# Optimization experiments

Hardware: AMD Instinct MI355X
Metric: run time of the kernel (lower is better)

## Reference

```python
import jax, jax.numpy as jnp
import numpy as np

IN_F, D_FC, D_H = 5, 32, 64

def setup_inputs() -> dict:
    key = jax.random.key(0)
    ks = jax.random.split(key, 10)
    B, T = 4096, 512
    s_fc = 1.0 / np.sqrt(IN_F)
    s_rnn = 1.0 / np.sqrt(D_H)
    s_out = 1.0 / np.sqrt(D_H)
    return {
        "x":    jax.random.normal(ks[0], (B, T, IN_F), dtype=jnp.float32),
        "W0":   jax.random.uniform(ks[1], (D_FC, IN_F), jnp.float32, -s_fc, s_fc),
        "b0":   jax.random.uniform(ks[2], (D_FC,), jnp.float32, -s_fc, s_fc),
        "W_ih": jax.random.uniform(ks[3], (4 * D_H, D_FC), jnp.float32, -s_rnn, s_rnn),
        "W_hh": jax.random.uniform(ks[4], (4 * D_H, D_H), jnp.float32, -s_rnn, s_rnn),
        "b_ih": jax.random.uniform(ks[5], (4 * D_H,), jnp.float32, -s_rnn, s_rnn),
        "b_hh": jax.random.uniform(ks[6], (4 * D_H,), jnp.float32, -s_rnn, s_rnn),
        "Wo":   jax.random.uniform(ks[7], (1, D_H), jnp.float32, -s_out, s_out),
        "bo":   jax.random.uniform(ks[8], (1,), jnp.float32, -s_out, s_out),
    }

def reference(x, W0, b0, W_ih, W_hh, b_ih, b_hh, Wo, bo):
    B, T, _ = x.shape
    # fc0: [B,T,5] -> [B,T,32]
    h0 = x @ W0.T + b0
    # Precompute input-side gate projections for all timesteps: [B,T,4H]
    xg = h0 @ W_ih.T + (b_ih + b_hh)
    xg_t = jnp.swapaxes(xg, 0, 1)  # [T,B,4H] for scan

    def step(carry, xg_step):
        h, c = carry
        gates = xg_step + h @ W_hh.T          # [B,4H]
        i, f, g, o = jnp.split(gates, 4, axis=-1)  # PyTorch gate order i,f,g,o
        i = jax.nn.sigmoid(i)
        f = jax.nn.sigmoid(f)
        g = jnp.tanh(g)
        o = jax.nn.sigmoid(o)
        c = f * c + i * g
        h = o * jnp.tanh(c)
        return (h, c), None

    init = (jnp.zeros((B, D_H), x.dtype), jnp.zeros((B, D_H), x.dtype))
    (h_last, _), _ = jax.lax.scan(step, init, xg_t)
    # out Linear on last timestep hidden: r_out[:, -1, :] == h_last
    return h_last @ Wo.T + bo  # [B,1]
```

## Files before the change

### kernel.cpp

```cpp
#include <hip/hip_runtime.h>

#define B_TOT   4096
#define T_STEPS 512
#define IN_F    5
#define D_FC    32
#define D_H     64
#define MB      16
#define NROW    16
#define ROWE    72

typedef _Float16 h8 __attribute__((ext_vector_type(8)));
typedef __fp16   h2 __attribute__((ext_vector_type(2)));
typedef float    f4 __attribute__((ext_vector_type(4)));

__device__ __forceinline__ float fexp2(float x) { return __builtin_amdgcn_exp2f(x); }
__device__ __forceinline__ float frcp(float x)  { return __builtin_amdgcn_rcpf(x); }

__global__ __launch_bounds__(256) void lstm_mfma(
    const float* __restrict__ x,
    const float* __restrict__ W0,
    const float* __restrict__ b0,
    const float* __restrict__ W_ih,
    const float* __restrict__ W_hh,
    const float* __restrict__ b_ih,
    const float* __restrict__ b_hh,
    const float* __restrict__ Wo,
    const float* __restrict__ bo,
    float* __restrict__ out)
{
    __shared__ __align__(16) _Float16 H[2][NROW][ROWE];

    const int tid  = threadIdx.x;
    const int lane = tid & 63;
    const int w    = tid >> 6;
    const int col  = lane & 15;
    const int quad = lane >> 4;
    const int bblk = blockIdx.x * MB;

    const float K1 = 1.4426950408889634f;
    const float K2 = 2.8853900817779268f;

    h8 Bf[4][2];
    #pragma unroll
    for (int q = 0; q < 4; ++q) {
        const int row = q * 64 + w * 16 + col;
        #pragma unroll
        for (int c = 0; c < 2; ++c) {
            h8 f;
            #pragma unroll
            for (int jj = 0; jj < 8; ++jj) {
                const int k = c * 32 + quad * 8 + jj;
                f[jj] = (_Float16)W_hh[row * D_H + k];
            }
            Bf[q][c] = f;
        }
    }

    h8 Bx[4];
    #pragma unroll
    for (int q = 0; q < 4; ++q) {
        const int row = q * 64 + w * 16 + col;
        h8 f;
        #pragma unroll
        for (int jj = 0; jj < 8; ++jj) f[jj] = (_Float16)0.0f;
        if (quad == 0) {
            #pragma unroll
            for (int jj = 0; jj < IN_F; ++jj) {
                float s = 0.0f;
                #pragma unroll
                for (int m = 0; m < D_FC; ++m)
                    s = fmaf(W_ih[row * D_FC + m], W0[m * IN_F + jj], s);
                f[jj] = (_Float16)s;
            }
        }
        Bx[q] = f;
    }

    float sb[4];
    #pragma unroll
    for (int q = 0; q < 4; ++q) {
        const int row = q * 64 + w * 16 + col;
        float s = b_ih[row] + b_hh[row];
        #pragma unroll
        for (int m = 0; m < D_FC; ++m)
            s = fmaf(W_ih[row * D_FC + m], b0[m], s);
        sb[q] = s;
    }
    const float nbi = -K1 * sb[0];
    const float nbf = -K1 * sb[1];
    const float pbg =  K2 * sb[2];
    const float nbo = -K1 * sb[3];

    for (int i = tid; i < 2 * NROW * ROWE; i += 256)
        ((_Float16*)H)[i] = (_Float16)0.0f;

    const float* xb = x + (size_t)(bblk + col) * T_STEPS * IN_F;

    union AxU { h8 v; h2 p[4]; };
    AxU Ax[2];
    #pragma unroll
    for (int jj = 0; jj < 8; ++jj) { Ax[0].v[jj] = (_Float16)0.0f; Ax[1].v[jj] = (_Float16)0.0f; }
    {
        const f4 v0 = *(const f4*)xb;
        const float s0 = xb[4];
        Ax[0].p[0] = __builtin_amdgcn_cvt_pkrtz(v0[0], v0[1]);
        Ax[0].p[1] = __builtin_amdgcn_cvt_pkrtz(v0[2], v0[3]);
        Ax[0].p[2] = __builtin_amdgcn_cvt_pkrtz(s0, 0.0f);
    }
    f4 xv[2]; float x4[2];
    xv[0] = *(const f4*)(xb + IN_F);      x4[0] = xb[IN_F + 4];
    xv[1] = *(const f4*)(xb + 2 * IN_F);  x4[1] = xb[2 * IN_F + 4];

    f4 zk = {0.0f, 0.0f, 0.0f, 0.0f};
    float cs[4] = {0.0f, 0.0f, 0.0f, 0.0f};

    __syncthreads();

    for (int it = 0; it < T_STEPS / 2; ++it) {
        #pragma unroll
        for (int u = 0; u < 2; ++u) {
            const h8 A1 = *(const h8*)&H[u][col][quad * 8];
            const h8 A2 = *(const h8*)&H[u][col][32 + quad * 8];

            Ax[u ^ 1].p[0] = __builtin_amdgcn_cvt_pkrtz(xv[u][0], xv[u][1]);
            Ax[u ^ 1].p[1] = __builtin_amdgcn_cvt_pkrtz(xv[u][2], xv[u][3]);
            Ax[u ^ 1].p[2] = __builtin_amdgcn_cvt_pkrtz(x4[u], 0.0f);
            {
                int tn = 2 * it + u + 3;
                tn = (tn < T_STEPS) ? tn : (T_STEPS - 1);
                const float* xp = xb + tn * IN_F;
                xv[u] = *(const f4*)xp;
                x4[u] = xp[4];
            }

            f4 acc[4];
            #pragma unroll
            for (int q = 0; q < 4; ++q) {
                f4 a = __builtin_amdgcn_mfma_f32_16x16x32_f16(Ax[u].v, Bx[q], zk, 0, 0, 0);
                a = __builtin_amdgcn_mfma_f32_16x16x32_f16(A1, Bf[q][0], a, 0, 0, 0);
                a = __builtin_amdgcn_mfma_f32_16x16x32_f16(A2, Bf[q][1], a, 0, 0, 0);
                acc[q] = a;
            }

            #pragma unroll
            for (int r = 0; r < 4; ++r) {
                const float ig = frcp(1.0f + fexp2(fmaf(-K1, acc[0][r], nbi)));
                const float fg = frcp(1.0f + fexp2(fmaf(-K1, acc[1][r], nbf)));
                const float eg = fexp2(fmaf(K2, acc[2][r], pbg));
                const float gg = fmaf(-2.0f, frcp(eg + 1.0f), 1.0f);
                const float og = frcp(1.0f + fexp2(fmaf(-K1, acc[3][r], nbo)));
                cs[r] = fmaf(fg, cs[r], ig * gg);
                const float ec = fexp2(K2 * cs[r]);
                const float th = fmaf(-2.0f, frcp(ec + 1.0f), 1.0f);
                H[u ^ 1][quad * 4 + r][w * 16 + col] = (_Float16)(og * th);
            }

            asm volatile("s_waitcnt lgkmcnt(0)" ::: "memory");
            __builtin_amdgcn_s_barrier();
            asm volatile("" ::: "memory");
        }
    }

    if (tid < MB) {
        float a = bo[0];
        #pragma unroll 8
        for (int j = 0; j < D_H; ++j)
            a = fmaf((float)H[0][tid][j], Wo[j], a);
        out[bblk + tid] = a;
    }
}

extern "C" void kernel_launch(void* const* d_in, const int* in_sizes, int n_in,
                              void* d_out, int out_size, void* d_ws, size_t ws_size,
                              hipStream_t stream) {
    const float* x    = (const float*)d_in[0];
    const float* W0   = (const float*)d_in[1];
    const float* b0   = (const float*)d_in[2];
    const float* W_ih = (const float*)d_in[3];
    const float* W_hh = (const float*)d_in[4];
    const float* b_ih = (const float*)d_in[5];
    const float* b_hh = (const float*)d_in[6];
    const float* Wo   = (const float*)d_in[7];
    const float* bo   = (const float*)d_in[8];
    float* out = (float*)d_out;

    hipLaunchKernelGGL(lstm_mfma, dim3(B_TOT / MB), dim3(256), 0, stream,
                       x, W0, b0, W_ih, W_hh, b_ih, b_hh, Wo, bo, out);
}
```

Measured before the change: 328.4 us.

## Split hidden-state K dimension across two wave halves with LDS partial-sum exchange

Doubles the block to 512 threads, so each gate column group is handled by two waves. Each wave does half of the K=64 recurrent MFMA reduction, and only the first half also does the input projection. The waves swap partial accumulators through a new shared buffer, and each computes the gate nonlinearities for two of the four output rows. The goal is to shorten the per-step serial MFMA chain and the activation work per wave. In exchange it adds an extra barrier and LDS traffic on every timestep.

```diff
diff --git a/kernel.cpp b/kernel.cpp
--- a/kernel.cpp
+++ b/kernel.cpp
@@ -16,7 +16,7 @@
 __device__ __forceinline__ float fexp2(float x) { return __builtin_amdgcn_exp2f(x); }
 __device__ __forceinline__ float frcp(float x)  { return __builtin_amdgcn_rcpf(x); }
 
-__global__ __launch_bounds__(256) void lstm_mfma(
+__global__ __launch_bounds__(512) void lstm_mfma(
     const float* __restrict__ x,
     const float* __restrict__ W0,
     const float* __restrict__ b0,
@@ -29,10 +29,13 @@
     float* __restrict__ out)
 {
     __shared__ __align__(16) _Float16 H[2][NROW][ROWE];
+    __shared__ __align__(16) float EX[2][4][64][8];
 
     const int tid  = threadIdx.x;
     const int lane = tid & 63;
     const int w    = tid >> 6;
+    const int p    = w & 3;
+    const int half = w >> 2;
     const int col  = lane & 15;
     const int quad = lane >> 4;
     const int bblk = blockIdx.x * MB;
@@ -40,46 +43,44 @@
     const float K1 = 1.4426950408889634f;
     const float K2 = 2.8853900817779268f;
 
-    h8 Bf[4][2];
+    h8 Bf[4];
     #pragma unroll
     for (int q = 0; q < 4; ++q) {
-        const int row = q * 64 + w * 16 + col;
-        #pragma unroll
-        for (int c = 0; c < 2; ++c) {
-            h8 f;
-            #pragma unroll
-            for (int jj = 0; jj < 8; ++jj) {
-                const int k = c * 32 + quad * 8 + jj;
-                f[jj] = (_Float16)W_hh[row * D_H + k];
-            }
-            Bf[q][c] = f;
+        const int row = q * 64 + p * 16 + col;
+        h8 f;
+        #pragma unroll
+        for (int jj = 0; jj < 8; ++jj) {
+            const int k = half * 32 + quad * 8 + jj;
+            f[jj] = (_Float16)W_hh[row * D_H + k];
         }
+        Bf[q] = f;
     }
 
     h8 Bx[4];
     #pragma unroll
     for (int q = 0; q < 4; ++q) {
-        const int row = q * 64 + w * 16 + col;
-        h8 f;
-        #pragma unroll
-        for (int jj = 0; jj < 8; ++jj) f[jj] = (_Float16)0.0f;
-        if (quad == 0) {
+        #pragma unroll
+        for (int jj = 0; jj < 8; ++jj) Bx[q][jj] = (_Float16)0.0f;
+    }
+    if (half == 0 && quad == 0) {
+        #pragma unroll
+        for (int q = 0; q < 4; ++q) {
+            const int row = q * 64 + p * 16 + col;
             #pragma unroll
             for (int jj = 0; jj < IN_F; ++jj) {
                 float s = 0.0f;
                 #pragma unroll
                 for (int m = 0; m < D_FC; ++m)
                     s = fmaf(W_ih[row * D_FC + m], W0[m * IN_F + jj], s);
-                f[jj] = (_Float16)s;
+                Bx[q][jj] = (_Float16)s;
             }
         }
-        Bx[q] = f;
     }
 
     float sb[4];
     #pragma unroll
     for (int q = 0; q < 4; ++q) {
-        const int row = q * 64 + w * 16 + col;
+        const int row = q * 64 + p * 16 + col;
         float s = b_ih[row] + b_hh[row];
         #pragma unroll
         for (int m = 0; m < D_FC; ++m)
@@ -91,41 +92,43 @@
     const float pbg =  K2 * sb[2];
     const float nbo = -K1 * sb[3];
 
-    for (int i = tid; i < 2 * NROW * ROWE; i += 256)
+    for (int i = tid; i < 2 * NROW * ROWE; i += 512)
         ((_Float16*)H)[i] = (_Float16)0.0f;
 
     const float* xb = x + (size_t)(bblk + col) * T_STEPS * IN_F;
 
-    union AxU { h8 v; h2 p[4]; };
+    union AxU { h8 v; h2 pk[4]; };
     AxU Ax[2];
     #pragma unroll
     for (int jj = 0; jj < 8; ++jj) { Ax[0].v[jj] = (_Float16)0.0f; Ax[1].v[jj] = (_Float16)0.0f; }
-    {
+    f4 xv[2]; float x4[2];
+    if (half == 0) {
         const f4 v0 = *(const f4*)xb;
         const float s0 = xb[4];
-        Ax[0].p[0] = __builtin_amdgcn_cvt_pkrtz(v0[0], v0[1]);
-        Ax[0].p[1] = __builtin_amdgcn_cvt_pkrtz(v0[2], v0[3]);
-        Ax[0].p[2] = __builtin_amdgcn_cvt_pkrtz(s0, 0.0f);
-    }
-    f4 xv[2]; float x4[2];
-    xv[0] = *(const f4*)(xb + IN_F);      x4[0] = xb[IN_F + 4];
-    xv[1] = *(const f4*)(xb + 2 * IN_F);  x4[1] = xb[2 * IN_F + 4];
+        Ax[0].pk[0] = __builtin_amdgcn_cvt_pkrtz(v0[0], v0[1]);
+        Ax[0].pk[1] = __builtin_amdgcn_cvt_pkrtz(v0[2], v0[3]);
+        Ax[0].pk[2] = __builtin_amdgcn_cvt_pkrtz(s0, 0.0f);
+        xv[0] = *(const f4*)(xb + IN_F);      x4[0] = xb[IN_F + 4];
+        xv[1] = *(const f4*)(xb + 2 * IN_F);  x4[1] = xb[2 * IN_F + 4];
+    }
 
     f4 zk = {0.0f, 0.0f, 0.0f, 0.0f};
-    float cs[4] = {0.0f, 0.0f, 0.0f, 0.0f};
+    float cs[2] = {0.0f, 0.0f};
+
+    float* const exw = &EX[half][p][lane][0];
+    const float* const exr = &EX[half ^ 1][p][lane][0];
 
     __syncthreads();
 
     for (int it = 0; it < T_STEPS / 2; ++it) {
         #pragma unroll
         for (int u = 0; u < 2; ++u) {
-            const h8 A1 = *(const h8*)&H[u][col][quad * 8];
-            const h8 A2 = *(const h8*)&H[u][col][32 + quad * 8];
-
-            Ax[u ^ 1].p[0] = __builtin_amdgcn_cvt_pkrtz(xv[u][0], xv[u][1]);
-            Ax[u ^ 1].p[1] = __builtin_amdgcn_cvt_pkrtz(xv[u][2], xv[u][3]);
-            Ax[u ^ 1].p[2] = __builtin_amdgcn_cvt_pkrtz(x4[u], 0.0f);
-            {
+            const h8 A = *(const h8*)&H[u][col][half * 32 + quad * 8];
+
+            if (half == 0) {
+                Ax[u ^ 1].pk[0] = __builtin_amdgcn_cvt_pkrtz(xv[u][0], xv[u][1]);
+                Ax[u ^ 1].pk[1] = __builtin_amdgcn_cvt_pkrtz(xv[u][2], xv[u][3]);
+                Ax[u ^ 1].pk[2] = __builtin_amdgcn_cvt_pkrtz(x4[u], 0.0f);
                 int tn = 2 * it + u + 3;
                 tn = (tn < T_STEPS) ? tn : (T_STEPS - 1);
                 const float* xp = xb + tn * IN_F;
@@ -134,25 +137,58 @@
             }
 
             f4 acc[4];
+            if (half == 0) {
+                #pragma unroll
+                for (int q = 0; q < 4; ++q) {
+                    f4 a = __builtin_amdgcn_mfma_f32_16x16x32_f16(Ax[u].v, Bx[q], zk, 0, 0, 0);
+                    a = __builtin_amdgcn_mfma_f32_16x16x32_f16(A, Bf[q], a, 0, 0, 0);
+                    acc[q] = a;
+                }
+            } else {
+                #pragma unroll
+                for (int q = 0; q < 4; ++q)
+                    acc[q] = __builtin_amdgcn_mfma_f32_16x16x32_f16(A, Bf[q], zk, 0, 0, 0);
+            }
+
+            float g0[4], g1[4];
+            f4 pk0, pk1;
+            if (half == 0) {
+                pk0 = (f4){acc[0][2], acc[1][2], acc[2][2], acc[3][2]};
+                pk1 = (f4){acc[0][3], acc[1][3], acc[2][3], acc[3][3]};
+                #pragma unroll
+                for (int q = 0; q < 4; ++q) { g0[q] = acc[q][0]; g1[q] = acc[q][1]; }
+            } else {
+                pk0 = (f4){acc[0][0], acc[1][0], acc[2][0], acc[3][0]};
+                pk1 = (f4){acc[0][1], acc[1][1], acc[2][1], acc[3][1]};
+                #pragma unroll
+                for (int q = 0; q < 4; ++q) { g0[q] = acc[q][2]; g1[q] = acc[q][3]; }
+            }
+            *(f4*)exw       = pk0;
+            *(f4*)(exw + 4) = pk1;
+
+            asm volatile("s_waitcnt lgkmcnt(0)" ::: "memory");
+            __builtin_amdgcn_s_barrier();
+            asm volatile("" ::: "memory");
+
+            const f4 rd0 = *(const f4*)exr;
+            const f4 rd1 = *(const f4*)(exr + 4);
+
             #pragma unroll
-            for (int q = 0; q < 4; ++q) {
-                f4 a = __builtin_amdgcn_mfma_f32_16x16x32_f16(Ax[u].v, Bx[q], zk, 0, 0, 0);
-                a = __builtin_amdgcn_mfma_f32_16x16x32_f16(A1, Bf[q][0], a, 0, 0, 0);
-                a = __builtin_amdgcn_mfma_f32_16x16x32_f16(A2, Bf[q][1], a, 0, 0, 0);
-                acc[q] = a;
-            }
-
-            #pragma unroll
-            for (int r = 0; r < 4; ++r) {
-                const float ig = frcp(1.0f + fexp2(fmaf(-K1, acc[0][r], nbi)));
-                const float fg = frcp(1.0f + fexp2(fmaf(-K1, acc[1][r], nbf)));
-                const float eg = fexp2(fmaf(K2, acc[2][r], pbg));
+            for (int rl = 0; rl < 2; ++rl) {
+                const f4 rd = rl ? rd1 : rd0;
+                const float vi = (rl ? g1[0] : g0[0]) + rd[0];
+                const float vf = (rl ? g1[1] : g0[1]) + rd[1];
+                const float vg = (rl ? g1[2] : g0[2]) + rd[2];
+                const float vo = (rl ? g1[3] : g0[3]) + rd[3];
+                const float ig = frcp(1.0f + fexp2(fmaf(-K1, vi, nbi)));
+                const float fg = frcp(1.0f + fexp2(fmaf(-K1, vf, nbf)));
+                const float eg = fexp2(fmaf(K2, vg, pbg));
                 const float gg = fmaf(-2.0f, frcp(eg + 1.0f), 1.0f);
-                const float og = frcp(1.0f + fexp2(fmaf(-K1, acc[3][r], nbo)));
-                cs[r] = fmaf(fg, cs[r], ig * gg);
-                const float ec = fexp2(K2 * cs[r]);
+                const float og = frcp(1.0f + fexp2(fmaf(-K1, vo, nbo)));
+                cs[rl] = fmaf(fg, cs[rl], ig * gg);
+                const float ec = fexp2(K2 * cs[rl]);
                 const float th = fmaf(-2.0f, frcp(ec + 1.0f), 1.0f);
-                H[u ^ 1][quad * 4 + r][w * 16 + col] = (_Float16)(og * th);
+                H[u ^ 1][quad * 4 + half * 2 + rl][p * 16 + col] = (_Float16)(og * th);
             }
 
             asm volatile("s_waitcnt lgkmcnt(0)" ::: "memory");
@@ -184,6 +220,6 @@
     const float* bo   = (const float*)d_in[8];
     float* out = (float*)d_out;
 
-    hipLaunchKernelGGL(lstm_mfma, dim3(B_TOT / MB), dim3(256), 0, stream,
+    hipLaunchKernelGGL(lstm_mfma, dim3(B_TOT / MB), dim3(512), 0, stream,
                        x, W0, b0, W_ih, W_hh, b_ih, b_hh, Wo, bo, out);
 }
```

Result: slower. 457.0 us (+39.2%).
